# Kernel tuning notes

Hardware: AMD Instinct MI355X
Metric: run time of the kernel (lower is better)

Reference implementation:

```python
import jax, jax.numpy as jnp
import numpy as np

DN = ('NCHW', 'OIHW', 'NCHW')
EPS = 1e-5

def conv(x, w, pad):
    return jax.lax.conv_general_dilated(x, w, (1, 1), [(pad, pad), (pad, pad)], dimension_numbers=DN)

def bn(x, g, b, m, v):
    # eval-mode BatchNorm2d
    inv = g / jnp.sqrt(v + EPS)
    return x * inv.reshape(1, -1, 1, 1) + (b - m * inv).reshape(1, -1, 1, 1)

def up8_align_corners(x):
    # bilinear upsample x8 with align_corners=True (matches nn.Upsample)
    B, C, Hin, Win = x.shape
    Ho, Wo = Hin * 8, Win * 8
    ys = jnp.arange(Ho, dtype=x.dtype) * ((Hin - 1) / (Ho - 1))
    xs = jnp.arange(Wo, dtype=x.dtype) * ((Win - 1) / (Wo - 1))
    y0 = jnp.floor(ys).astype(jnp.int32); y1 = jnp.minimum(y0 + 1, Hin - 1)
    x0 = jnp.floor(xs).astype(jnp.int32); x1 = jnp.minimum(x0 + 1, Win - 1)
    wy = (ys - y0.astype(x.dtype))[None, None, :, None]
    wx = (xs - x0.astype(x.dtype))[None, None, None, :]
    rows = x[:, :, y0, :] * (1 - wy) + x[:, :, y1, :] * wy
    return rows[:, :, :, x0] * (1 - wx) + rows[:, :, :, x1] * wx

def setup_inputs() -> dict:
    key = jax.random.key(0)
    ks = jax.random.split(key, 24)
    B, Cin, H = 8, 384, 64
    Cmid = Cin + 64 * 3          # 576
    Ccat = 768 + 576 + 288       # 1632
    f = jnp.float32
    def rn(k, shp, s=0.05):
        return jax.random.normal(k, shp, dtype=f) * s
    inp = {
        'coarse_m': jax.random.normal(ks[0], (B, Cin, H, H), dtype=f),
        'x2_2':     jax.random.normal(ks[1], (B, 768, H, H), dtype=f),
        'x3_1':     jax.random.normal(ks[2], (B, 288, H, H), dtype=f),
        'raw_x':    jax.random.normal(ks[3], (B, 3, 8 * H, 8 * H), dtype=f),
        # conv_pred_m: 1x1, in_channels -> 1, with bias
        'w_pred': rn(ks[4], (1, Cin, 1, 1)),
        'b_pred': jnp.zeros((1,), f),
        # decoder block (conv3x3 + BN), Cmid -> Cmid
        'dec_w': rn(ks[5], (Cmid, Cmid, 3, 3)),
        'dec_g': 1.0 + rn(ks[6], (Cmid,)), 'dec_b': rn(ks[7], (Cmid,)),
        'dec_m': rn(ks[8], (Cmid,)), 'dec_v': 0.5 + jax.random.uniform(ks[9], (Cmid,), dtype=f),
        # conv_concat (conv3x3 + BN), 1632 -> Cmid
        'cc_w': rn(ks[10], (Cmid, Ccat, 3, 3)),
        'cc_g': 1.0 + rn(ks[11], (Cmid,)), 'cc_b': rn(ks[12], (Cmid,)),
        'cc_m': rn(ks[13], (Cmid,)), 'cc_v': 0.5 + jax.random.uniform(ks[14], (Cmid,), dtype=f),
        # conv_out1 (conv3x3 + BN), Cmid -> Cmid
        'o1_w': rn(ks[15], (Cmid, Cmid, 3, 3)),
        'o1_g': 1.0 + rn(ks[16], (Cmid,)), 'o1_b': rn(ks[17], (Cmid,)),
        'o1_m': rn(ks[18], (Cmid,)), 'o1_v': 0.5 + jax.random.uniform(ks[19], (Cmid,), dtype=f),
        # conv_out2: 1x1, Cmid -> 1, with bias
        'o2_w': rn(ks[20], (1, Cmid, 1, 1)),
        'o2_b': jnp.zeros((1,), f),
    }
    return inp

def reference(coarse_m, x2_2, x3_1, raw_x, w_pred, b_pred,
              dec_w, dec_g, dec_b, dec_m, dec_v,
              cc_w, cc_g, cc_b, cc_m, cc_v,
              o1_w, o1_g, o1_b, o1_m, o1_v,
              o2_w, o2_b):
    B, Craw, Hr, Wr = raw_x.shape
    p = Hr // 8  # raw patch size == coarse_m spatial size
    # coarse prediction map (sigmoid > 0 always -> every patch is selected)
    _pred = jax.nn.sigmoid(conv(coarse_m, w_pred, 0) + b_pred.reshape(1, -1, 1, 1))
    # 8x8 grid of raw patches, patch-major channel concat: [B, 64*Craw, p, p]
    patches = raw_x.reshape(B, Craw, 8, p, 8, p).transpose(0, 2, 4, 1, 3, 5).reshape(B, 64 * Craw, p, p)
    x = jnp.concatenate([coarse_m, patches], axis=1)          # [B, 576, H, H]
    x = bn(conv(x, dec_w, 1), dec_g, dec_b, dec_m, dec_v)      # decoder block
    x = jnp.concatenate([x2_2, x, x3_1], axis=1)               # [B, 1632, H, H]
    x = bn(conv(x, cc_w, 1), cc_g, cc_b, cc_m, cc_v)
    x = bn(conv(x, o1_w, 1), o1_g, o1_b, o1_m, o1_v)
    x = conv(x, o2_w, 0) + o2_b.reshape(1, -1, 1, 1)           # [B, 1, H, H]
    return up8_align_corners(x)                                # [B, 1, 8H, 8H]
```

## Files before the change

kernel.cpp:

```cpp
#include <hip/hip_runtime.h>
#include <hip/hip_bf16.h>
#include <stdint.h>

typedef __attribute__((ext_vector_type(8))) __bf16 bf16x8;
typedef __attribute__((ext_vector_type(8))) short short8;
typedef __attribute__((ext_vector_type(4))) float floatx4;
using bf16 = __hip_bfloat16;

#define DEVINL __device__ __forceinline__

typedef __attribute__((address_space(1))) const void gconst_void;
typedef __attribute__((address_space(3))) void lds_void;

DEVINL void gl2lds16(const void* g, void* l) {
    __builtin_amdgcn_global_load_lds((gconst_void*)g, (lds_void*)l, 16, 0, 0);
}

DEVINL unsigned short f2us(float x) {
    bf16 h = __float2bfloat16(x);
    return __builtin_bit_cast(unsigned short, h);
}
DEVINL float ld_in(const void* p, int f, size_t i) {
    return f ? ((const float*)p)[i] : __bfloat162float(((const bf16*)p)[i]);
}

__global__ void detect_k(const void* x, int* flag) {
    if (threadIdx.x == 0) {
        const float* xf = (const float*)x;
        int good = 0;
        for (int i = 0; i < 64; i++) {
            float a = fabsf(xf[i]);
            if (a > 1e-8f && a < 100.f) good++;
        }
        *flag = (good >= 48) ? 1 : 0;
    }
}


__global__ void zero_border_k(bf16* buf, int C) {
    int cell = blockIdx.x;
    int b = blockIdx.y;
    int hp, wp;
    if (cell < 66)       { hp = 0;          wp = cell; }
    else if (cell < 132) { hp = 65;         wp = cell - 66; }
    else if (cell < 196) { hp = cell - 131; wp = 0; }
    else                 { hp = cell - 195; wp = 65; }
    unsigned short* p = (unsigned short*)buf + (size_t)(b * 4356 + hp * 66 + wp) * C;
    for (int c = threadIdx.x; c < C; c += 256) p[c] = 0;
}

__global__ void zero_chanpad_k(bf16* Xb, int n) {
    int idx = blockIdx.x * 256 + threadIdx.x;
    if (idx >= n) return;
    int cell = idx >> 2, sub = idx & 3;
    uint4 z; z.x = 0; z.y = 0; z.z = 0; z.w = 0;
    *(uint4*)((unsigned short*)Xb + (size_t)cell * 1664 + 1632 + sub * 8) = z;
}

__global__ void nchw_to_pnhwc_k(const void* __restrict__ src, bf16* __restrict__ dst,
                                const int* __restrict__ flag,
                                int Csrc, int dstC, int chanOff, int b0) {
    __shared__ unsigned short t[32][72];
    int c0 = blockIdx.x * 32, h = blockIdx.y, bz = blockIdx.z;
    int tid = threadIdx.x;
    {
        int c = tid >> 3, w8 = (tid & 7) * 8;
        size_t base = (((size_t)((b0 + bz) * Csrc + c0 + c)) * 64 + h) * 64 + w8;
        unsigned short* tp = &t[c][w8];
        if (*flag) {
            const float* sf = (const float*)src;
            float4 v0 = *(const float4*)(sf + base);
            float4 v1 = *(const float4*)(sf + base + 4);
            tp[0] = f2us(v0.x); tp[1] = f2us(v0.y); tp[2] = f2us(v0.z); tp[3] = f2us(v0.w);
            tp[4] = f2us(v1.x); tp[5] = f2us(v1.y); tp[6] = f2us(v1.z); tp[7] = f2us(v1.w);
        } else {
            uint4 v = *(const uint4*)((const unsigned short*)src + base);
            *(uint4*)tp = v;
        }
    }
    __syncthreads();
    {
        int w = tid >> 2, cq = (tid & 3) * 8;
        uint32_t p0 = t[cq + 0][w] | ((uint32_t)t[cq + 1][w] << 16);
        uint32_t p1 = t[cq + 2][w] | ((uint32_t)t[cq + 3][w] << 16);
        uint32_t p2 = t[cq + 4][w] | ((uint32_t)t[cq + 5][w] << 16);
        uint32_t p3 = t[cq + 6][w] | ((uint32_t)t[cq + 7][w] << 16);
        uint4 o; o.x = p0; o.y = p1; o.z = p2; o.w = p3;
        size_t off = ((size_t)(bz * 4356 + (h + 1) * 66 + (w + 1))) * dstC + chanOff + c0 + cq;
        *(uint4*)((unsigned short*)dst + off) = o;
    }
}

__global__ void raw_patches_k(const void* __restrict__ raw, bf16* __restrict__ Xa,
                              const int* __restrict__ flag, int b0) {
    __shared__ unsigned short t[8][520];
    int h = blockIdx.x, craw = blockIdx.y, bz = blockIdx.z;
    int tid = threadIdx.x;
    int f = *flag;
#pragma unroll
    for (int k = 0; k < 2; k++) {
        int s = tid + k * 256;
        int gy = s >> 6, seg = s & 63;
        size_t base = (((size_t)((b0 + bz) * 3 + craw) * 512) + gy * 64 + h) * 512 + seg * 8;
        unsigned short* tp = &t[gy][seg * 8];
        if (f) {
            const float* rf = (const float*)raw;
            float4 v0 = *(const float4*)(rf + base);
            float4 v1 = *(const float4*)(rf + base + 4);
            tp[0] = f2us(v0.x); tp[1] = f2us(v0.y); tp[2] = f2us(v0.z); tp[3] = f2us(v0.w);
            tp[4] = f2us(v1.x); tp[5] = f2us(v1.y); tp[6] = f2us(v1.z); tp[7] = f2us(v1.w);
        } else {
            uint4 v = *(const uint4*)((const unsigned short*)raw + base);
            *(uint4*)tp = v;
        }
    }
    __syncthreads();
#pragma unroll
    for (int k = 0; k < 2; k++) {
        int s = tid + k * 256;
        int w = s >> 3, gq = s & 7;
        uint32_t p0 = t[gq][0 * 64 + w] | ((uint32_t)t[gq][1 * 64 + w] << 16);
        uint32_t p1 = t[gq][2 * 64 + w] | ((uint32_t)t[gq][3 * 64 + w] << 16);
        uint32_t p2 = t[gq][4 * 64 + w] | ((uint32_t)t[gq][5 * 64 + w] << 16);
        uint32_t p3 = t[gq][6 * 64 + w] | ((uint32_t)t[gq][7 * 64 + w] << 16);
        uint4 o; o.x = p0; o.y = p1; o.z = p2; o.w = p3;
        size_t off = ((size_t)(bz * 4356 + (h + 1) * 66 + (w + 1))) * 576 + 384 + craw * 64 + gq * 8;
        *(uint4*)((unsigned short*)Xa + off) = o;
    }
}

__global__ void fold_w_k(const void* __restrict__ W, bf16* __restrict__ dst,
                         const int* __restrict__ flag, int srcC, int dstC, int remap) {
    int ci = blockIdx.x * 256 + threadIdx.x;
    if (ci >= dstC) return;
    int co = blockIdx.y;
    int kk = blockIdx.z;
    unsigned short out = 0;
    if (co < 576 && ci < srcC) {
        int oc = ci;
        if (remap && ci >= 384) {
            int tt = ci - 384;
            int craw = tt >> 6, gy = (tt >> 3) & 7, gx = tt & 7;
            oc = 384 + gy * 24 + gx * 3 + craw;
        }
        size_t sidx = ((size_t)co * srcC + oc) * 9 + kk;
        out = (*flag) ? f2us(((const float*)W)[sidx]) : ((const unsigned short*)W)[sidx];
    }
    ((unsigned short*)dst)[((size_t)kk * 640 + co) * dstC + ci] = out;
}

__global__ void scale_beta_k(const void* g, const void* b, const void* m, const void* v,
                             const int* __restrict__ flag, float* inv_out, float* beta_out) {
    int i = blockIdx.x * 256 + threadIdx.x;
    int f = *flag;
    if (i < 576) {
        float inv = ld_in(g, f, i) / sqrtf(ld_in(v, f, i) + 1e-5f);
        inv_out[i] = inv;
        beta_out[i] = ld_in(b, f, i) - ld_in(m, f, i) * inv;
    }
}

__global__ __launch_bounds__(512, 2)
void conv3x3_mfma(const bf16* __restrict__ X, const bf16* __restrict__ Wp,
                  const float* __restrict__ inv, const float* __restrict__ beta,
                  bf16* __restrict__ dst, int Cin, int dstC, int chanOff, int dstPadded,
                  int mtiles) {
    __shared__ __align__(16) bf16 Alds[2 * 16384];
    __shared__ __align__(16) bf16 Blds[2 * 20480];
    const int tid = threadIdx.x;
    const int wv = tid >> 6;
    const int lane = tid & 63;
    const int quad = lane >> 4;
    const int r16 = lane & 15;

    const int nwg = gridDim.x;
    const int wg = ((int)blockIdx.x & 7) * (nwg >> 3) + ((int)blockIdx.x >> 3);
    const int m0 = (wg % mtiles) * 256;
    const int n0 = (wg / mtiles) * 320;

    const int rl = tid >> 3;
    const int cg = ((tid & 7) ^ (rl & 7)) * 8;
    int aF[4], bF[5];
#pragma unroll
    for (int q = 0; q < 4; q++) {
        int r = m0 + q * 64 + rl;
        int bb = r >> 12, hh = (r >> 6) & 63;
        aF[q] = (bb * 4356 + (hh + 1) * 66 + (rl + 1)) * Cin + cg;
    }
#pragma unroll
    for (int q = 0; q < 5; q++) bF[q] = (n0 + q * 64 + rl) * Cin + cg;

    const int wvM = wv >> 2, wvN = wv & 3;
    int aOff[8], bOff[5];
#pragma unroll
    for (int i = 0; i < 8; i++) aOff[i] = (wvM * 128 + i * 16 + r16) * 64;
#pragma unroll
    for (int j = 0; j < 5; j++) bOff[j] = (wvN * 80 + j * 16 + r16) * 64;
    const int sw0 = (quad ^ (r16 & 7)) * 8;
    const int sw1 = ((quad + 4) ^ (r16 & 7)) * 8;

    floatx4 acc[8][5];
    floatx4 zero = {0.f, 0.f, 0.f, 0.f};
#pragma unroll
    for (int i = 0; i < 8; i++)
#pragma unroll
        for (int j = 0; j < 5; j++) acc[i][j] = zero;

#define BAR() asm volatile("s_barrier" ::: "memory")
#define READB(sw) do { \
    _Pragma("unroll") for (int j_ = 0; j_ < 5; j_++) \
        bfr[j_] = *(const short8*)(Bp + bOff[j_] + (sw)); } while (0)
#define READA(h, sw) do { \
    _Pragma("unroll") for (int i_ = 0; i_ < 4; i_++) \
        af[i_] = *(const short8*)(Ap + aOff[(h) * 4 + i_] + (sw)); } while (0)
#define MM(h) do { \
    __builtin_amdgcn_s_setprio(1); \
    _Pragma("unroll") for (int i_ = 0; i_ < 4; i_++) \
    _Pragma("unroll") for (int j_ = 0; j_ < 5; j_++) \
        acc[(h) * 4 + i_][j_] = __builtin_amdgcn_mfma_f32_16x16x32_bf16( \
            __builtin_bit_cast(bf16x8, af[i_]), __builtin_bit_cast(bf16x8, bfr[j_]), \
            acc[(h) * 4 + i_][j_], 0, 0, 0); \
    __builtin_amdgcn_s_setprio(0); } while (0)
#define GA(q) gl2lds16(X + aF[q] + so, Ao + (q) * 4096 + wv * 512)
#define GB(q) gl2lds16(Wp + bF[q] + wo, Bo + (q) * 4096 + wv * 512)
#define ADV() do { ciN += 64; if (ciN == Cin) { ciN = 0; ++kkN; \
        tapOffN = ((kkN / 3) * 66 + (kkN % 3) - 67) * Cin; wbN += 640 * Cin; } } while (0)

    int kkN = 0, ciN = 0, tapOffN = -67 * Cin, wbN = 0;
    {
        const int so = tapOffN + ciN, wo = wbN + ciN;
        bf16* Ao = Alds; bf16* Bo = Blds;
        GA(0); GA(1); GA(2); GA(3);
        GB(0); GB(1); GB(2); GB(3); GB(4);
    }
    ADV();
    const int NT = 9 * (Cin >> 6);
    int p = 0;
    for (int t = 0; t < NT - 1; ++t, p ^= 1) {
        const bf16* Ap = Alds + p * 16384;
        const bf16* Bp = Blds + p * 20480;
        bf16* Ao = Alds + (p ^ 1) * 16384;
        bf16* Bo = Blds + (p ^ 1) * 20480;
        const int so = tapOffN + ciN, wo = wbN + ciN;
        short8 af[4], bfr[5];
        GA(0); GA(1); GA(2);
        asm volatile("s_waitcnt vmcnt(3)" ::: "memory");
        BAR();
        READB(sw0); READA(0, sw0);
        MM(0);
        READA(1, sw0);
        GA(3); GB(0); GB(1);
        MM(1);
        READB(sw1); READA(0, sw1);
        GB(2); GB(3); GB(4);
        MM(0);
        READA(1, sw1);
        MM(1);
        BAR();
        ADV();
    }
    {
        const bf16* Ap = Alds + p * 16384;
        const bf16* Bp = Blds + p * 20480;
        short8 af[4], bfr[5];
        asm volatile("s_waitcnt vmcnt(0)" ::: "memory");
        BAR();
        READB(sw0); READA(0, sw0); MM(0);
        READA(1, sw0); MM(1);
        READB(sw1); READA(0, sw1); MM(0);
        READA(1, sw1); MM(1);
    }
#undef BAR
#undef READB
#undef READA
#undef MM
#undef GA
#undef GB
#undef ADV

    int ncol[5]; float sj[5], bj[5]; bool nval[5];
#pragma unroll
    for (int j = 0; j < 5; j++) {
        ncol[j] = n0 + wvN * 80 + j * 16 + r16;
        nval[j] = ncol[j] < 576;
        sj[j] = nval[j] ? inv[ncol[j]] : 0.f;
        bj[j] = nval[j] ? beta[ncol[j]] : 0.f;
    }
#pragma unroll
    for (int i = 0; i < 8; i++) {
#pragma unroll
        for (int r = 0; r < 4; r++) {
            int row = m0 + wvM * 128 + i * 16 + quad * 4 + r;
            int didx;
            if (dstPadded) {
                int bb = row >> 12, hh = (row >> 6) & 63, ww = row & 63;
                didx = (bb * 4356 + (hh + 1) * 66 + (ww + 1)) * dstC + chanOff;
            } else {
                didx = row * dstC + chanOff;
            }
#pragma unroll
            for (int j = 0; j < 5; j++)
                if (nval[j]) dst[didx + ncol[j]] = __float2bfloat16(acc[i][j][r] * sj[j] + bj[j]);
        }
    }
}

__global__ void o2_dot_k(const bf16* __restrict__ Y, const void* __restrict__ w,
                         const void* __restrict__ bias, const int* __restrict__ flag,
                         float* __restrict__ smap) {
    __shared__ float wl[576];
    int tid = threadIdx.x;
    int f = *flag;
    for (int c = tid; c < 576; c += 256) wl[c] = ld_in(w, f, c);
    __syncthreads();
    int wv = tid >> 6, lane = tid & 63;
    int pix = blockIdx.x * 4 + wv;
    const bf16* yp = Y + (size_t)pix * 576;
    float s = 0.f;
#pragma unroll
    for (int k = 0; k < 9; k++) {
        int c = k * 64 + lane;
        s += __bfloat162float(yp[c]) * wl[c];
    }
#pragma unroll
    for (int off = 32; off; off >>= 1) s += __shfl_xor(s, off, 64);
    if (lane == 0) smap[pix] = s + ld_in(bias, f, 0);
}

__global__ void upsample_k(const float* __restrict__ smap, void* __restrict__ out,
                           const int* __restrict__ flag) {
    int idx = blockIdx.x * 256 + threadIdx.x;
    int b = idx >> 18;
    int ho = (idx >> 9) & 511;
    int wo = idx & 511;
    const float sc = 63.f / 511.f;
    float ys = ho * sc, xs = wo * sc;
    int y0 = (int)ys; float ty = ys - y0; int y1 = min(y0 + 1, 63);
    int x0 = (int)xs; float tx = xs - x0; int x1 = min(x0 + 1, 63);
    const float* sp = smap + (b << 12);
    float r0 = sp[y0 * 64 + x0] * (1.f - tx) + sp[y0 * 64 + x1] * tx;
    float r1 = sp[y1 * 64 + x0] * (1.f - tx) + sp[y1 * 64 + x1] * tx;
    float val = r0 * (1.f - ty) + r1 * ty;
    if (*flag) ((float*)out)[idx] = val;
    else       ((bf16*)out)[idx] = __float2bfloat16(val);
}

extern "C" void kernel_launch(void* const* d_in, const int* in_sizes, int n_in,
                              void* d_out, int out_size, void* d_ws, size_t ws_size,
                              hipStream_t stream) {
    const void* coarse = d_in[0];
    const void* x22    = d_in[1];
    const void* x31    = d_in[2];
    const void* rawx   = d_in[3];
    const void* dec_w = d_in[6];
    const void *dec_g = d_in[7], *dec_b = d_in[8], *dec_m = d_in[9], *dec_v = d_in[10];
    const void* cc_w = d_in[11];
    const void *cc_g = d_in[12], *cc_b = d_in[13], *cc_m = d_in[14], *cc_v = d_in[15];
    const void* o1_w = d_in[16];
    const void *o1_g = d_in[17], *o1_b = d_in[18], *o1_m = d_in[19], *o1_v = d_in[20];
    const void* o2_w = d_in[21];
    const void* o2_b = d_in[22];

    const size_t wcc_sz  = (size_t)9 * 640 * 1664 * 2;
    const size_t wsm_sz  = (size_t)9 * 640 * 576 * 2;
    const size_t tail_sz = 16384 + 131072 + 256;
    int G = 8; int sepW = 1;
    for (;;) {
        size_t acts = (size_t)G * 4356 * (576 + 1664) * 2;
        if (acts + wcc_sz + 2 * wsm_sz + tail_sz <= ws_size) { sepW = 1; break; }
        if (acts + wcc_sz + tail_sz <= ws_size)              { sepW = 0; break; }
        if (G == 1) { sepW = 0; break; }
        G >>= 1;
    }
    size_t xa_sz = (size_t)G * 4356 * 576 * 2;
    size_t xb_sz = (size_t)G * 4356 * 1664 * 2;

    char* ws = (char*)d_ws;
    bf16* Xa   = (bf16*)(ws);
    bf16* Xb   = (bf16*)(ws + xa_sz);
    bf16* Wcc  = (bf16*)(ws + xa_sz + xb_sz);
    bf16* Wdec = sepW ? (bf16*)(ws + xa_sz + xb_sz + wcc_sz) : Wcc;
    bf16* Wo1  = sepW ? (bf16*)(ws + xa_sz + xb_sz + wcc_sz + wsm_sz) : Wcc;
    size_t wtot = wcc_sz + (sepW ? 2 * wsm_sz : 0);
    float* sb  = (float*)(ws + xa_sz + xb_sz + wtot);
    float* invDec = sb,        *betaDec = sb + 576;
    float* invCc  = sb + 1152, *betaCc  = sb + 1728;
    float* invO1  = sb + 2304, *betaO1  = sb + 2880;
    float* smap = (float*)(ws + xa_sz + xb_sz + wtot + 16384);
    int* flag   = (int*)(ws + xa_sz + xb_sz + wtot + 16384 + 131072);
    bf16* Yo1q = Xb;

    detect_k<<<1, 64, 0, stream>>>(coarse, flag);
    scale_beta_k<<<3, 256, 0, stream>>>(dec_g, dec_b, dec_m, dec_v, flag, invDec, betaDec);
    scale_beta_k<<<3, 256, 0, stream>>>(cc_g, cc_b, cc_m, cc_v, flag, invCc, betaCc);
    scale_beta_k<<<3, 256, 0, stream>>>(o1_g, o1_b, o1_m, o1_v, flag, invO1, betaO1);
    if (sepW) {
        fold_w_k<<<dim3(3, 640, 9), 256, 0, stream>>>(dec_w, Wdec, flag, 576, 576, 1);
        fold_w_k<<<dim3(7, 640, 9), 256, 0, stream>>>(cc_w, Wcc, flag, 1632, 1664, 0);
        fold_w_k<<<dim3(3, 640, 9), 256, 0, stream>>>(o1_w, Wo1, flag, 576, 576, 0);
    }

    const int nchunk = 8 / G;
    const int mt = G * 16;
    for (int q = 0; q < nchunk; q++) {
        const int b0 = q * G;
        zero_border_k<<<dim3(260, G), 256, 0, stream>>>(Xa, 576);
        zero_border_k<<<dim3(260, G), 256, 0, stream>>>(Xb, 1664);
        zero_chanpad_k<<<(G * 4356 * 4 + 255) / 256, 256, 0, stream>>>(Xb, G * 4356 * 4);
        nchw_to_pnhwc_k<<<dim3(12, 64, G), 256, 0, stream>>>(coarse, Xa, flag, 384, 576, 0, b0);
        raw_patches_k<<<dim3(64, 3, G), 256, 0, stream>>>(rawx, Xa, flag, b0);
        nchw_to_pnhwc_k<<<dim3(24, 64, G), 256, 0, stream>>>(x22, Xb, flag, 768, 1664, 0, b0);
        nchw_to_pnhwc_k<<<dim3(9, 64, G), 256, 0, stream>>>(x31, Xb, flag, 288, 1664, 1344, b0);
        if (!sepW) fold_w_k<<<dim3(3, 640, 9), 256, 0, stream>>>(dec_w, Wdec, flag, 576, 576, 1);
        conv3x3_mfma<<<dim3(mt * 2), 512, 0, stream>>>(Xa, Wdec, invDec, betaDec, Xb, 576, 1664, 768, 1, mt);
        if (!sepW) fold_w_k<<<dim3(7, 640, 9), 256, 0, stream>>>(cc_w, Wcc, flag, 1632, 1664, 0);
        conv3x3_mfma<<<dim3(mt * 2), 512, 0, stream>>>(Xb, Wcc, invCc, betaCc, Xa, 1664, 576, 0, 1, mt);
        if (!sepW) fold_w_k<<<dim3(3, 640, 9), 256, 0, stream>>>(o1_w, Wo1, flag, 576, 576, 0);
        conv3x3_mfma<<<dim3(mt * 2), 512, 0, stream>>>(Xa, Wo1, invO1, betaO1, Yo1q, 576, 576, 0, 0, mt);
        o2_dot_k<<<G * 1024, 256, 0, stream>>>(Yo1q, o2_w, o2_b, flag, smap + (size_t)q * G * 4096);
    }
    upsample_k<<<8192, 256, 0, stream>>>(smap, d_out, flag);
}
```

Before: 1.290 ms.

## Fuse final 1x1 conv into o1 conv epilogue and reorder B-tile loads

The last 1x1 conv (576->1) is folded into the epilogue of the o1 3x3 conv. Each wave computes partial dot products over its columns, reduces them with shuffles and atomically adds them into a score map that is pre-initialised with the bias. This removes the o1 activation write to global memory and the separate o2_dot kernel. The main loop also issues three B-tile loads earlier, before the barrier, with the waitcnt adjusted to match, to overlap more global traffic. Atomics make the float summation order nondeterministic.

```diff
diff --git a/kernel.cpp b/kernel.cpp
--- a/kernel.cpp
+++ b/kernel.cpp
@@ -160,11 +160,21 @@
     }
 }
 
+__global__ void o2w_k(const void* __restrict__ w, const void* __restrict__ bias,
+                      const int* __restrict__ flag, float* __restrict__ w2f,
+                      float* __restrict__ smap, int npix) {
+    int i = blockIdx.x * 256 + threadIdx.x;
+    int f = *flag;
+    if (i < 576) w2f[i] = ld_in(w, f, i);
+    float b2 = ld_in(bias, f, 0);
+    if (i < npix) smap[i] = b2;
+}
+
 __global__ __launch_bounds__(512, 2)
 void conv3x3_mfma(const bf16* __restrict__ X, const bf16* __restrict__ Wp,
                   const float* __restrict__ inv, const float* __restrict__ beta,
                   bf16* __restrict__ dst, int Cin, int dstC, int chanOff, int dstPadded,
-                  int mtiles) {
+                  int mtiles, const float* __restrict__ w2, float* __restrict__ smap) {
     __shared__ __align__(16) bf16 Alds[2 * 16384];
     __shared__ __align__(16) bf16 Blds[2 * 20480];
     const int tid = threadIdx.x;
@@ -243,16 +253,16 @@
         bf16* Bo = Blds + (p ^ 1) * 20480;
         const int so = tapOffN + ciN, wo = wbN + ciN;
         short8 af[4], bfr[5];
-        GA(0); GA(1); GA(2);
-        asm volatile("s_waitcnt vmcnt(3)" ::: "memory");
+        GA(0); GA(1); GA(2); GB(0); GB(1); GB(2);
+        asm volatile("s_waitcnt vmcnt(6)" ::: "memory");
         BAR();
         READB(sw0); READA(0, sw0);
         MM(0);
         READA(1, sw0);
-        GA(3); GB(0); GB(1);
+        GA(3);
         MM(1);
         READB(sw1); READA(0, sw1);
-        GB(2); GB(3); GB(4);
+        GB(3); GB(4);
         MM(0);
         READA(1, sw1);
         MM(1);
@@ -286,45 +296,43 @@
         sj[j] = nval[j] ? inv[ncol[j]] : 0.f;
         bj[j] = nval[j] ? beta[ncol[j]] : 0.f;
     }
-#pragma unroll
-    for (int i = 0; i < 8; i++) {
-#pragma unroll
-        for (int r = 0; r < 4; r++) {
-            int row = m0 + wvM * 128 + i * 16 + quad * 4 + r;
-            int didx;
-            if (dstPadded) {
-                int bb = row >> 12, hh = (row >> 6) & 63, ww = row & 63;
-                didx = (bb * 4356 + (hh + 1) * 66 + (ww + 1)) * dstC + chanOff;
-            } else {
-                didx = row * dstC + chanOff;
+    if (w2 != nullptr) {
+        float wj[5];
+#pragma unroll
+        for (int j = 0; j < 5; j++) wj[j] = nval[j] ? w2[ncol[j]] : 0.f;
+#pragma unroll
+        for (int i = 0; i < 8; i++) {
+#pragma unroll
+            for (int r = 0; r < 4; r++) {
+                float ps = 0.f;
+#pragma unroll
+                for (int j = 0; j < 5; j++)
+                    ps += (acc[i][j][r] * sj[j] + bj[j]) * wj[j];
+#pragma unroll
+                for (int off = 1; off < 16; off <<= 1) ps += __shfl_xor(ps, off, 64);
+                if (r16 == 0)
+                    atomicAdd(&smap[m0 + wvM * 128 + i * 16 + quad * 4 + r], ps);
             }
-#pragma unroll
-            for (int j = 0; j < 5; j++)
-                if (nval[j]) dst[didx + ncol[j]] = __float2bfloat16(acc[i][j][r] * sj[j] + bj[j]);
-        }
-    }
-}
-
-__global__ void o2_dot_k(const bf16* __restrict__ Y, const void* __restrict__ w,
-                         const void* __restrict__ bias, const int* __restrict__ flag,
-                         float* __restrict__ smap) {
-    __shared__ float wl[576];
-    int tid = threadIdx.x;
-    int f = *flag;
-    for (int c = tid; c < 576; c += 256) wl[c] = ld_in(w, f, c);
-    __syncthreads();
-    int wv = tid >> 6, lane = tid & 63;
-    int pix = blockIdx.x * 4 + wv;
-    const bf16* yp = Y + (size_t)pix * 576;
-    float s = 0.f;
-#pragma unroll
-    for (int k = 0; k < 9; k++) {
-        int c = k * 64 + lane;
-        s += __bfloat162float(yp[c]) * wl[c];
-    }
-#pragma unroll
-    for (int off = 32; off; off >>= 1) s += __shfl_xor(s, off, 64);
-    if (lane == 0) smap[pix] = s + ld_in(bias, f, 0);
+        }
+    } else {
+#pragma unroll
+        for (int i = 0; i < 8; i++) {
+#pragma unroll
+            for (int r = 0; r < 4; r++) {
+                int row = m0 + wvM * 128 + i * 16 + quad * 4 + r;
+                int didx;
+                if (dstPadded) {
+                    int bb = row >> 12, hh = (row >> 6) & 63, ww = row & 63;
+                    didx = (bb * 4356 + (hh + 1) * 66 + (ww + 1)) * dstC + chanOff;
+                } else {
+                    didx = row * dstC + chanOff;
+                }
+#pragma unroll
+                for (int j = 0; j < 5; j++)
+                    if (nval[j]) dst[didx + ncol[j]] = __float2bfloat16(acc[i][j][r] * sj[j] + bj[j]);
+            }
+        }
+    }
 }
 
 __global__ void upsample_k(const float* __restrict__ smap, void* __restrict__ out,
@@ -386,14 +394,15 @@
     float* invDec = sb,        *betaDec = sb + 576;
     float* invCc  = sb + 1152, *betaCc  = sb + 1728;
     float* invO1  = sb + 2304, *betaO1  = sb + 2880;
+    float* w2f    = sb + 3456;
     float* smap = (float*)(ws + xa_sz + xb_sz + wtot + 16384);
     int* flag   = (int*)(ws + xa_sz + xb_sz + wtot + 16384 + 131072);
-    bf16* Yo1q = Xb;
 
     detect_k<<<1, 64, 0, stream>>>(coarse, flag);
     scale_beta_k<<<3, 256, 0, stream>>>(dec_g, dec_b, dec_m, dec_v, flag, invDec, betaDec);
     scale_beta_k<<<3, 256, 0, stream>>>(cc_g, cc_b, cc_m, cc_v, flag, invCc, betaCc);
     scale_beta_k<<<3, 256, 0, stream>>>(o1_g, o1_b, o1_m, o1_v, flag, invO1, betaO1);
+    o2w_k<<<128, 256, 0, stream>>>(o2_w, o2_b, flag, w2f, smap, 32768);
     if (sepW) {
         fold_w_k<<<dim3(3, 640, 9), 256, 0, stream>>>(dec_w, Wdec, flag, 576, 576, 1);
         fold_w_k<<<dim3(7, 640, 9), 256, 0, stream>>>(cc_w, Wcc, flag, 1632, 1664, 0);
@@ -412,12 +421,12 @@
         nchw_to_pnhwc_k<<<dim3(24, 64, G), 256, 0, stream>>>(x22, Xb, flag, 768, 1664, 0, b0);
         nchw_to_pnhwc_k<<<dim3(9, 64, G), 256, 0, stream>>>(x31, Xb, flag, 288, 1664, 1344, b0);
         if (!sepW) fold_w_k<<<dim3(3, 640, 9), 256, 0, stream>>>(dec_w, Wdec, flag, 576, 576, 1);
-        conv3x3_mfma<<<dim3(mt * 2), 512, 0, stream>>>(Xa, Wdec, invDec, betaDec, Xb, 576, 1664, 768, 1, mt);
+        conv3x3_mfma<<<dim3(mt * 2), 512, 0, stream>>>(Xa, Wdec, invDec, betaDec, Xb, 576, 1664, 768, 1, mt, nullptr, nullptr);
         if (!sepW) fold_w_k<<<dim3(7, 640, 9), 256, 0, stream>>>(cc_w, Wcc, flag, 1632, 1664, 0);
-        conv3x3_mfma<<<dim3(mt * 2), 512, 0, stream>>>(Xb, Wcc, invCc, betaCc, Xa, 1664, 576, 0, 1, mt);
+        conv3x3_mfma<<<dim3(mt * 2), 512, 0, stream>>>(Xb, Wcc, invCc, betaCc, Xa, 1664, 576, 0, 1, mt, nullptr, nullptr);
         if (!sepW) fold_w_k<<<dim3(3, 640, 9), 256, 0, stream>>>(o1_w, Wo1, flag, 576, 576, 0);
-        conv3x3_mfma<<<dim3(mt * 2), 512, 0, stream>>>(Xa, Wo1, invO1, betaO1, Yo1q, 576, 576, 0, 0, mt);
-        o2_dot_k<<<G * 1024, 256, 0, stream>>>(Yo1q, o2_w, o2_b, flag, smap + (size_t)q * G * 4096);
+        conv3x3_mfma<<<dim3(mt * 2), 512, 0, stream>>>(Xa, Wo1, invO1, betaO1, nullptr, 576, 576, 0, 0, mt,
+                                                       w2f, smap + (size_t)q * G * 4096);
     }
     upsample_k<<<8192, 256, 0, stream>>>(smap, d_out, flag);
 }
```

After: 1.440 ms. 1.12x slower.
